# Kernel optimization log

Hardware: AMD Instinct MI355X
Metric: run time of the kernel (lower is better)

## Reference

```python
import jax, jax.numpy as jnp
import numpy as np

B, C_FEAT, C_COND, C_KEY, H, W = 4, 256, 256, 32, 64, 64


def setup_inputs() -> dict:
    key = jax.random.key(0)
    ks = jax.random.split(key, 8)
    s = 0.02
    return {
        "features": jax.random.normal(ks[0], (B, C_FEAT, H, W), jnp.float32),
        "conditions": jax.random.normal(ks[1], (B, C_COND, H, W), jnp.float32),
        "Wq": jax.random.normal(ks[2], (C_KEY, C_COND), jnp.float32) * s,
        "bq": jnp.zeros((C_KEY,), jnp.float32),
        "Wk": jax.random.normal(ks[3], (C_KEY, C_FEAT), jnp.float32) * s,
        "bk": jnp.zeros((C_KEY,), jnp.float32),
        "Wv": jax.random.normal(ks[4], (C_FEAT, C_FEAT), jnp.float32) * s,
        "bv": jnp.zeros((C_FEAT,), jnp.float32),
        "gamma": jnp.zeros((1,), jnp.float32),
    }


def reference(features, conditions, Wq, bq, Wk, bk, Wv, bv, gamma):
    b, c, h, w = features.shape
    n = h * w
    feat = features.reshape(b, c, n)            # [B, C, N]
    cond = conditions.reshape(b, cond_c := conditions.shape[1], n)
    # 1x1 convs == per-pixel linear projections
    q = jnp.einsum('kc,bcn->bnk', Wq, cond) + bq          # [B, N, Ck]
    k = jnp.einsum('kc,bcn->bkn', Wk, feat) + bk[:, None]  # [B, Ck, N]
    v = jnp.einsum('oc,bcn->bon', Wv, feat) + bv[:, None]  # [B, C, N]
    energy = jnp.einsum('bik,bkj->bij', q, k)             # [B, N, N]
    attn = jax.nn.softmax(energy, axis=-1)
    out = jnp.einsum('bcj,bij->bci', v, attn)             # [B, C, N]
    out = out.reshape(b, c, h, w)
    return gamma * out + features
```

## Files before the change

### kernel.cpp

```cpp
#include <hip/hip_runtime.h>

typedef __bf16 bf16_t;
typedef __bf16 bf16x2 __attribute__((ext_vector_type(2)));
typedef __bf16 bf16x4 __attribute__((ext_vector_type(4)));
typedef __bf16 bf16x8 __attribute__((ext_vector_type(8)));
typedef float f32x4 __attribute__((ext_vector_type(4)));
typedef unsigned u32;
typedef unsigned u32x4 __attribute__((ext_vector_type(4)));

#define N_PIX 4096
#define CFEAT 256
#define CKEY 32
#define NBATCH 4

#if __has_builtin(__builtin_amdgcn_exp2f)
#define EXP2(x) __builtin_amdgcn_exp2f(x)
#else
#define EXP2(x) exp2f(x)
#endif

static __device__ __forceinline__ f32x4 mfma16(bf16x8 a, bf16x8 b, f32x4 c) {
    return __builtin_amdgcn_mfma_f32_16x16x32_bf16(a, b, c, 0, 0, 0);
}

static __device__ __forceinline__ void glds16(const void* g, void* l) {
    __builtin_amdgcn_global_load_lds(
        (const __attribute__((address_space(1))) void*)g,
        (__attribute__((address_space(3))) void*)l, 16, 0, 0);
}

static __device__ __forceinline__ u32 pk2(float lo, float hi) {
    bf16x2 t; t[0] = (bf16_t)lo; t[1] = (bf16_t)hi;
    return __builtin_bit_cast(u32, t);
}

static __device__ __forceinline__ void xpose4(u32 &x, u32 &y) {
#if __has_builtin(__builtin_amdgcn_permlane32_swap) && __has_builtin(__builtin_amdgcn_permlane16_swap)
    auto r32 = __builtin_amdgcn_permlane32_swap(x, y, false, false);
    auto r16 = __builtin_amdgcn_permlane16_swap(r32[0], r32[1], false, false);
    x = r16[0]; y = r16[1];
#else
    const int lane = threadIdx.x & 63;
    const int g = lane >> 4, ln = lane & 15;
    const int i0 = ln + ((g & 1) << 5);
    const int i2 = i0 + 16;
    u32 xs0 = (u32)__shfl((int)x, i0), ys0 = (u32)__shfl((int)y, i0);
    u32 xs2 = (u32)__shfl((int)x, i2), ys2 = (u32)__shfl((int)y, i2);
    x = (g < 2) ? xs0 : ys0;
    y = (g < 2) ? xs2 : ys2;
#endif
}

static __device__ __forceinline__ void softmax_tile(
    const bf16x8 kf[4], bf16x8 qf, bool addl,
    float &ls0, float &ls1, float &ls2, float &ls3,
    bf16x8 &pa0, bf16x8 &pa1)
{
    f32x4 zero = {0.f, 0.f, 0.f, 0.f};
    f32x4 st[4];
#pragma unroll
    for (int jt = 0; jt < 4; ++jt) st[jt] = mfma16(kf[jt], qf, zero);
    float ex[16];
#pragma unroll
    for (int jt = 0; jt < 4; ++jt)
#pragma unroll
        for (int r = 0; r < 4; ++r) ex[jt * 4 + r] = EXP2(st[jt][r]);
    if (addl) {
#pragma unroll
        for (int t = 0; t < 16; t += 4) {
            ls0 += ex[t]; ls1 += ex[t + 1]; ls2 += ex[t + 2]; ls3 += ex[t + 3];
        }
    }
    u32 a0 = pk2(ex[0],  ex[1]),  a1 = pk2(ex[2],  ex[3]);
    u32 b0 = pk2(ex[4],  ex[5]),  b1 = pk2(ex[6],  ex[7]);
    u32 c0 = pk2(ex[8],  ex[9]),  c1 = pk2(ex[10], ex[11]);
    u32 d0 = pk2(ex[12], ex[13]), d1 = pk2(ex[14], ex[15]);
    xpose4(a0, b0); xpose4(a1, b1);
    xpose4(c0, d0); xpose4(c1, d1);
    u32x4 w0 = {a0, a1, b0, b1};
    u32x4 w1 = {c0, c1, d0, d1};
    pa0 = __builtin_bit_cast(bf16x8, w0);
    pa1 = __builtin_bit_cast(bf16x8, w1);
}

__global__ __launch_bounds__(256) void projqk_kernel(
    const float* __restrict__ Wq, const float* __restrict__ bq, const float* __restrict__ Xq,
    const float* __restrict__ Wk, const float* __restrict__ bk, const float* __restrict__ Xk,
    bf16_t* __restrict__ Qt, bf16_t* __restrict__ Kt)
{
    __shared__ __attribute__((aligned(16))) bf16_t T[64][40];
    const int lane = threadIdx.x & 63, wave = threadIdx.x >> 6;
    const int g = lane >> 4, ln = lane & 15;
    const bool isK = (blockIdx.y == 1);
    const float* W    = isK ? Wk : Wq;
    const float* bias = isK ? bk : bq;
    const float* X  = (isK ? Xk : Xq) + (size_t)blockIdx.z * CFEAT * N_PIX;
    bf16_t*      Yt = (isK ? Kt : Qt) + (size_t)blockIdx.z * N_PIX * CKEY;
    const float qscale = isK ? 1.0f : 1.4426950408889634f;

    const int m_base = (wave & 1) * 16;
    const int n_loc  = (wave >> 1) * 32;
    const int n_base = blockIdx.x * 64 + n_loc;

    f32x4 zero = {0.f, 0.f, 0.f, 0.f};
    f32x4 acc[2] = {zero, zero};
    for (int k0 = 0; k0 < CFEAT; k0 += 32) {
        bf16x8 a;
        const float* wp = W + (size_t)(m_base + ln) * CFEAT + k0 + g * 8;
#pragma unroll
        for (int j = 0; j < 8; ++j) a[j] = (bf16_t)wp[j];
#pragma unroll
        for (int nt = 0; nt < 2; ++nt) {
            const float* xp = X + (size_t)(k0 + g * 8) * N_PIX + n_base + nt * 16 + ln;
            bf16x8 bfr;
#pragma unroll
            for (int j = 0; j < 8; ++j) bfr[j] = (bf16_t)xp[(size_t)j * N_PIX];
            acc[nt] = mfma16(a, bfr, acc[nt]);
        }
    }
#pragma unroll
    for (int nt = 0; nt < 2; ++nt)
#pragma unroll
        for (int r = 0; r < 4; ++r) {
            const int ck = m_base + g * 4 + r;
            T[n_loc + nt * 16 + ln][ck] = (bf16_t)((acc[nt][r] + bias[ck]) * qscale);
        }
    __syncthreads();
    const int n  = threadIdx.x >> 2;
    const int sg = threadIdx.x & 3;
    bf16x8 row = *(const bf16x8*)&T[n][sg * 8];
    *(bf16x8*)&Yt[(size_t)(blockIdx.x * 64 + n) * CKEY + sg * 8] = row;
}

__global__ __launch_bounds__(256, 4) void projv_kernel(
    const float* __restrict__ W, const float* __restrict__ bias,
    const float* __restrict__ X, bf16_t* __restrict__ V)
{
    const int lane = threadIdx.x & 63, wave = threadIdx.x >> 6;
    const int g = lane >> 4, ln = lane & 15;
    const int b = blockIdx.z;
    const int n_base = blockIdx.x * 32;
    const int c_wave = blockIdx.y * 128 + wave * 32;
    const float* Xb = X + (size_t)b * CFEAT * N_PIX;
    bf16_t*      Vb = V + (size_t)b * CFEAT * N_PIX;

    f32x4 zero = {0.f, 0.f, 0.f, 0.f};
    f32x4 acc[2][2];
#pragma unroll
    for (int mt = 0; mt < 2; ++mt) { acc[mt][0] = zero; acc[mt][1] = zero; }

    for (int k0 = 0; k0 < CFEAT; k0 += 32) {
        bf16x8 bfr[2];
#pragma unroll
        for (int nt = 0; nt < 2; ++nt) {
            const float* xp = Xb + (size_t)(k0 + g * 8) * N_PIX + n_base + nt * 16 + ln;
#pragma unroll
            for (int j = 0; j < 8; ++j) bfr[nt][j] = (bf16_t)xp[(size_t)j * N_PIX];
        }
#pragma unroll
        for (int mt = 0; mt < 2; ++mt) {
            const float* wp = W + (size_t)(c_wave + mt * 16 + ln) * CFEAT + k0 + g * 8;
            bf16x8 a;
#pragma unroll
            for (int j = 0; j < 8; ++j) a[j] = (bf16_t)wp[j];
            acc[mt][0] = mfma16(a, bfr[0], acc[mt][0]);
            acc[mt][1] = mfma16(a, bfr[1], acc[mt][1]);
        }
    }
#pragma unroll
    for (int mt = 0; mt < 2; ++mt)
#pragma unroll
        for (int nt = 0; nt < 2; ++nt)
#pragma unroll
            for (int r = 0; r < 4; ++r) {
                const int m = c_wave + mt * 16 + g * 4 + r;
                const int n = n_base + nt * 16 + ln;
                Vb[(size_t)m * N_PIX + n] = (bf16_t)(acc[mt][nt][r] + bias[m]);
            }
}

__global__ __launch_bounds__(256, 4) void pv_kernel(
    const bf16_t* __restrict__ Qt, const bf16_t* __restrict__ Kt,
    const bf16_t* __restrict__ V,
    const float* __restrict__ features, const float* __restrict__ gamma,
    float* __restrict__ out)
{
    __shared__ __attribute__((aligned(16))) bf16_t Vlds[4][64 * 64];

    const int lane = threadIdx.x & 63, wave = threadIdx.x >> 6;
    const int g = lane >> 4, ln = lane & 15;
    const int b = blockIdx.z;
    const int i_base = blockIdx.y * 64 + wave * 16;
    const int c_base = blockIdx.x * 64;

    const bf16_t* Qb = Qt + (size_t)b * N_PIX * CKEY;
    const bf16_t* Kb = Kt + (size_t)b * N_PIX * CKEY;
    const bf16_t* Vb = V + (size_t)b * CFEAT * N_PIX;

    const int s0 = wave * 128 + lane;
    const int s1 = s0 + 64;
    const int sc0 = s0 >> 3, sj0 = (s0 & 7) ^ (sc0 & 7);
    const int sc1 = s1 >> 3, sj1 = (s1 & 7) ^ (sc1 & 7);
    const bf16_t* vg0 = Vb + (size_t)(c_base + sc0) * N_PIX + sj0 * 8;
    const bf16_t* vg1 = Vb + (size_t)(c_base + sc1) * N_PIX + sj1 * 8;

    const bf16x8 qf = *(const bf16x8*)&Qb[(size_t)(i_base + ln) * CKEY + g * 8];

    f32x4 zero = {0.f, 0.f, 0.f, 0.f};
    f32x4 acc[4] = {zero, zero, zero, zero};
    float ls0 = 0.f, ls1 = 0.f, ls2 = 0.f, ls3 = 0.f;

    bf16x8 pa0c, pa1c;
    {
        bf16x8 kf[4];
#pragma unroll
        for (int jt = 0; jt < 4; ++jt)
            kf[jt] = *(const bf16x8*)&Kb[(size_t)(jt * 16 + ln) * CKEY + g * 8];
        asm volatile("" ::: "memory");
        glds16(vg0,      &Vlds[0][wave * 1024]);
        glds16(vg1,      &Vlds[0][wave * 1024 + 512]);
        glds16(vg0 + 64, &Vlds[1][wave * 1024]);
        glds16(vg1 + 64, &Vlds[1][wave * 1024 + 512]);
        softmax_tile(kf, qf, true, ls0, ls1, ls2, ls3, pa0c, pa1c);
        asm volatile("s_waitcnt vmcnt(2)" ::: "memory");
        __builtin_amdgcn_s_barrier();
        asm volatile("" ::: "memory");
    }

    for (int n = 0; n < 64; ++n) {
        const bf16_t* Vt = &Vlds[n & 3][0];
        bf16x8 vf[8];
#pragma unroll
        for (int ct = 0; ct < 4; ++ct) {
            const int c = ct * 16 + ln;
            vf[2 * ct]     = *(const bf16x8*)&Vt[(c * 8 + ( g      ^ (c & 7))) * 8];
            vf[2 * ct + 1] = *(const bf16x8*)&Vt[(c * 8 + ((4 + g) ^ (c & 7))) * 8];
        }

        const int jq = ((n + 1) & 63) * 64;
        bf16x8 kf[4];
#pragma unroll
        for (int jt = 0; jt < 4; ++jt)
            kf[jt] = *(const bf16x8*)&Kb[(size_t)(jq + jt * 16 + ln) * CKEY + g * 8];
        asm volatile("" ::: "memory");

        const int jn = (n * 64 + 128) & (N_PIX - 1);
        bf16_t* ldst = &Vlds[(n + 2) & 3][wave * 1024];
        glds16(vg0 + jn, ldst);
        glds16(vg1 + jn, ldst + 512);

        bf16x8 pa0n, pa1n;
        softmax_tile(kf, qf, n < 63, ls0, ls1, ls2, ls3, pa0n, pa1n);

        asm volatile("s_waitcnt vmcnt(2)" ::: "memory");
        __builtin_amdgcn_s_barrier();
        asm volatile("" ::: "memory");

#pragma unroll
        for (int ct = 0; ct < 4; ++ct) {
            acc[ct] = mfma16(vf[2 * ct],     pa0c, acc[ct]);
            acc[ct] = mfma16(vf[2 * ct + 1], pa1c, acc[ct]);
        }
        pa0c = pa0n; pa1c = pa1n;
    }

    float lsum = (ls0 + ls1) + (ls2 + ls3);
    lsum += __shfl_xor(lsum, 16);
    lsum += __shfl_xor(lsum, 32);
    const float s_lane = gamma[0] / lsum;

#pragma unroll
    for (int ct = 0; ct < 4; ++ct)
#pragma unroll
        for (int r = 0; r < 4; ++r) {
            const int c = c_base + ct * 16 + g * 4 + r;
            const int i = i_base + ln;
            const size_t idx = ((size_t)b * CFEAT + c) * N_PIX + i;
            out[idx] = s_lane * acc[ct][r] + features[idx];
        }
}

extern "C" void kernel_launch(void* const* d_in, const int* in_sizes, int n_in,
                              void* d_out, int out_size, void* d_ws, size_t ws_size,
                              hipStream_t stream) {
    const float* features   = (const float*)d_in[0];
    const float* conditions = (const float*)d_in[1];
    const float* Wq  = (const float*)d_in[2];
    const float* bq  = (const float*)d_in[3];
    const float* Wk  = (const float*)d_in[4];
    const float* bk  = (const float*)d_in[5];
    const float* Wv  = (const float*)d_in[6];
    const float* bv  = (const float*)d_in[7];
    const float* gam = (const float*)d_in[8];
    float* out = (float*)d_out;

    bf16_t* Qt = (bf16_t*)d_ws;
    bf16_t* Kt = Qt + (size_t)NBATCH * N_PIX * CKEY;
    bf16_t* Vw = Kt + (size_t)NBATCH * N_PIX * CKEY;

    projqk_kernel<<<dim3(N_PIX / 64, 2, NBATCH), 256, 0, stream>>>(
        Wq, bq, conditions, Wk, bk, features, Qt, Kt);
    projv_kernel<<<dim3(N_PIX / 32, 2, NBATCH), 256, 0, stream>>>(Wv, bv, features, Vw);
    pv_kernel<<<dim3(4, N_PIX / 64, NBATCH), 256, 0, stream>>>(
        Qt, Kt, Vw, features, gam, out);
}
```

Measured before the change: 193.0 us.

## Widen PV channel tile to 128, compute row sums via MFMA, double-buffer K loads

Each pv_kernel block now covers 128 channels instead of 64. This halves the number of blocks that recompute the QK^T energies and the exp for the same rows, and the launch grid is halved to match. The softmax denominator now comes from an MFMA against a ones vector on the bf16-packed probabilities rather than scalar float adds. The main loop is unrolled by two, with ping-pong K fragment registers prefetched two tiles ahead. In exchange, register and LDS use double (launch bounds drop to 2 waves per SIMD), and the row sums now use bf16-rounded values.

Measured after the change: 172.8 us. 10.4% less time.

```diff
diff --git a/kernel.cpp b/kernel.cpp
--- a/kernel.cpp
+++ b/kernel.cpp
@@ -52,9 +52,8 @@
 }
 
 static __device__ __forceinline__ void softmax_tile(
-    const bf16x8 kf[4], bf16x8 qf, bool addl,
-    float &ls0, float &ls1, float &ls2, float &ls3,
-    bf16x8 &pa0, bf16x8 &pa1)
+    const bf16x8 kf[4], bf16x8 qf, bf16x8 ones,
+    f32x4 &accsum, bf16x8 &pa0, bf16x8 &pa1)
 {
     f32x4 zero = {0.f, 0.f, 0.f, 0.f};
     f32x4 st[4];
@@ -65,12 +64,6 @@
     for (int jt = 0; jt < 4; ++jt)
 #pragma unroll
         for (int r = 0; r < 4; ++r) ex[jt * 4 + r] = EXP2(st[jt][r]);
-    if (addl) {
-#pragma unroll
-        for (int t = 0; t < 16; t += 4) {
-            ls0 += ex[t]; ls1 += ex[t + 1]; ls2 += ex[t + 2]; ls3 += ex[t + 3];
-        }
-    }
     u32 a0 = pk2(ex[0],  ex[1]),  a1 = pk2(ex[2],  ex[3]);
     u32 b0 = pk2(ex[4],  ex[5]),  b1 = pk2(ex[6],  ex[7]);
     u32 c0 = pk2(ex[8],  ex[9]),  c1 = pk2(ex[10], ex[11]);
@@ -81,6 +74,8 @@
     u32x4 w1 = {c0, c1, d0, d1};
     pa0 = __builtin_bit_cast(bf16x8, w0);
     pa1 = __builtin_bit_cast(bf16x8, w1);
+    accsum = mfma16(ones, pa0, accsum);
+    accsum = mfma16(ones, pa1, accsum);
 }
 
 __global__ __launch_bounds__(256) void projqk_kernel(
@@ -179,98 +174,128 @@
             }
 }
 
-__global__ __launch_bounds__(256, 4) void pv_kernel(
+__global__ __launch_bounds__(256, 2) void pv_kernel(
     const bf16_t* __restrict__ Qt, const bf16_t* __restrict__ Kt,
     const bf16_t* __restrict__ V,
     const float* __restrict__ features, const float* __restrict__ gamma,
     float* __restrict__ out)
 {
-    __shared__ __attribute__((aligned(16))) bf16_t Vlds[4][64 * 64];
+    __shared__ __attribute__((aligned(16))) bf16_t Vlds[4][128 * 64];
 
     const int lane = threadIdx.x & 63, wave = threadIdx.x >> 6;
     const int g = lane >> 4, ln = lane & 15;
     const int b = blockIdx.z;
     const int i_base = blockIdx.y * 64 + wave * 16;
-    const int c_base = blockIdx.x * 64;
+    const int c_base = blockIdx.x * 128;
 
     const bf16_t* Qb = Qt + (size_t)b * N_PIX * CKEY;
     const bf16_t* Kb = Kt + (size_t)b * N_PIX * CKEY;
     const bf16_t* Vb = V + (size_t)b * CFEAT * N_PIX;
 
-    const int s0 = wave * 128 + lane;
-    const int s1 = s0 + 64;
+    const int s0 = wave * 256 + lane, s1 = s0 + 64, s2 = s0 + 128, s3 = s0 + 192;
     const int sc0 = s0 >> 3, sj0 = (s0 & 7) ^ (sc0 & 7);
     const int sc1 = s1 >> 3, sj1 = (s1 & 7) ^ (sc1 & 7);
+    const int sc2 = s2 >> 3, sj2 = (s2 & 7) ^ (sc2 & 7);
+    const int sc3 = s3 >> 3, sj3 = (s3 & 7) ^ (sc3 & 7);
     const bf16_t* vg0 = Vb + (size_t)(c_base + sc0) * N_PIX + sj0 * 8;
     const bf16_t* vg1 = Vb + (size_t)(c_base + sc1) * N_PIX + sj1 * 8;
+    const bf16_t* vg2 = Vb + (size_t)(c_base + sc2) * N_PIX + sj2 * 8;
+    const bf16_t* vg3 = Vb + (size_t)(c_base + sc3) * N_PIX + sj3 * 8;
 
     const bf16x8 qf = *(const bf16x8*)&Qb[(size_t)(i_base + ln) * CKEY + g * 8];
 
+    bf16x8 ones;
+#pragma unroll
+    for (int j = 0; j < 8; ++j) ones[j] = (bf16_t)1.0f;
+
     f32x4 zero = {0.f, 0.f, 0.f, 0.f};
-    f32x4 acc[4] = {zero, zero, zero, zero};
-    float ls0 = 0.f, ls1 = 0.f, ls2 = 0.f, ls3 = 0.f;
-
+    f32x4 acc[8] = {zero, zero, zero, zero, zero, zero, zero, zero};
+    f32x4 accsum = zero;
+
+    bf16x8 kfA[4], kfB[4];
     bf16x8 pa0c, pa1c;
+
     {
-        bf16x8 kf[4];
+        bf16x8 kf0[4];
 #pragma unroll
         for (int jt = 0; jt < 4; ++jt)
-            kf[jt] = *(const bf16x8*)&Kb[(size_t)(jt * 16 + ln) * CKEY + g * 8];
+            kf0[jt] = *(const bf16x8*)&Kb[(size_t)(jt * 16 + ln) * CKEY + g * 8];
         asm volatile("" ::: "memory");
-        glds16(vg0,      &Vlds[0][wave * 1024]);
-        glds16(vg1,      &Vlds[0][wave * 1024 + 512]);
-        glds16(vg0 + 64, &Vlds[1][wave * 1024]);
-        glds16(vg1 + 64, &Vlds[1][wave * 1024 + 512]);
-        softmax_tile(kf, qf, true, ls0, ls1, ls2, ls3, pa0c, pa1c);
-        asm volatile("s_waitcnt vmcnt(2)" ::: "memory");
+        glds16(vg0, &Vlds[0][wave * 2048]);
+        glds16(vg1, &Vlds[0][wave * 2048 + 512]);
+        glds16(vg2, &Vlds[0][wave * 2048 + 1024]);
+        glds16(vg3, &Vlds[0][wave * 2048 + 1536]);
+        glds16(vg0 + 64, &Vlds[1][wave * 2048]);
+        glds16(vg1 + 64, &Vlds[1][wave * 2048 + 512]);
+        glds16(vg2 + 64, &Vlds[1][wave * 2048 + 1024]);
+        glds16(vg3 + 64, &Vlds[1][wave * 2048 + 1536]);
+#pragma unroll
+        for (int jt = 0; jt < 4; ++jt)
+            kfA[jt] = *(const bf16x8*)&Kb[(size_t)(64 + jt * 16 + ln) * CKEY + g * 8];
+        softmax_tile(kf0, qf, ones, accsum, pa0c, pa1c);
+        asm volatile("s_waitcnt vmcnt(8)" ::: "memory");
         __builtin_amdgcn_s_barrier();
         asm volatile("" ::: "memory");
     }
 
-    for (int n = 0; n < 64; ++n) {
-        const bf16_t* Vt = &Vlds[n & 3][0];
-        bf16x8 vf[8];
-#pragma unroll
-        for (int ct = 0; ct < 4; ++ct) {
-            const int c = ct * 16 + ln;
-            vf[2 * ct]     = *(const bf16x8*)&Vt[(c * 8 + ( g      ^ (c & 7))) * 8];
-            vf[2 * ct + 1] = *(const bf16x8*)&Vt[(c * 8 + ((4 + g) ^ (c & 7))) * 8];
-        }
-
-        const int jq = ((n + 1) & 63) * 64;
-        bf16x8 kf[4];
-#pragma unroll
-        for (int jt = 0; jt < 4; ++jt)
-            kf[jt] = *(const bf16x8*)&Kb[(size_t)(jq + jt * 16 + ln) * CKEY + g * 8];
-        asm volatile("" ::: "memory");
-
-        const int jn = (n * 64 + 128) & (N_PIX - 1);
-        bf16_t* ldst = &Vlds[(n + 2) & 3][wave * 1024];
-        glds16(vg0 + jn, ldst);
-        glds16(vg1 + jn, ldst + 512);
-
-        bf16x8 pa0n, pa1n;
-        softmax_tile(kf, qf, n < 63, ls0, ls1, ls2, ls3, pa0n, pa1n);
-
-        asm volatile("s_waitcnt vmcnt(2)" ::: "memory");
-        __builtin_amdgcn_s_barrier();
-        asm volatile("" ::: "memory");
-
-#pragma unroll
-        for (int ct = 0; ct < 4; ++ct) {
-            acc[ct] = mfma16(vf[2 * ct],     pa0c, acc[ct]);
-            acc[ct] = mfma16(vf[2 * ct + 1], pa1c, acc[ct]);
-        }
-        pa0c = pa0n; pa1c = pa1n;
+#define PV_ITER(NN, KFU, KFN)                                                  \
+  {                                                                            \
+    const int nn = (NN);                                                       \
+    const bf16_t* Vt = &Vlds[nn & 3][0];                                       \
+    bf16x8 vfl[8];                                                             \
+    _Pragma("unroll")                                                          \
+    for (int ct = 0; ct < 4; ++ct) {                                           \
+      const int c = ct * 16 + ln;                                              \
+      vfl[2 * ct]     = *(const bf16x8*)&Vt[(c * 8 + ( g      ^ (c & 7))) * 8];\
+      vfl[2 * ct + 1] = *(const bf16x8*)&Vt[(c * 8 + ((4 + g) ^ (c & 7))) * 8];\
+    }                                                                          \
+    const int jq2 = ((nn + 2) & 63) * 64;                                      \
+    _Pragma("unroll")                                                          \
+    for (int jt = 0; jt < 4; ++jt)                                             \
+      KFN[jt] = *(const bf16x8*)&Kb[(size_t)(jq2 + jt * 16 + ln) * CKEY + g * 8]; \
+    asm volatile("" ::: "memory");     \
+    const int jn = (nn * 64 + 128) & (N_PIX - 1);                              \
+    bf16_t* ldst = &Vlds[(nn + 2) & 3][wave * 2048];                           \
+    glds16(vg0 + jn, ldst);                                                    \
+    glds16(vg1 + jn, ldst + 512);                                              \
+    glds16(vg2 + jn, ldst + 1024);                                             \
+    glds16(vg3 + jn, ldst + 1536);                                             \
+    bf16x8 pa0n, pa1n;                                                         \
+    const bool live = (nn < 63);                                               \
+    if (live) softmax_tile(KFU, qf, ones, accsum, pa0n, pa1n);                 \
+    asm volatile("s_waitcnt vmcnt(8)" ::: "memory");                           \
+    __builtin_amdgcn_s_barrier();                                              \
+    asm volatile("" ::: "memory");                                             \
+    bf16x8 vfh[8];                                                             \
+    _Pragma("unroll")                                                          \
+    for (int ct = 4; ct < 8; ++ct) {                                           \
+      const int c = ct * 16 + ln;                                              \
+      vfh[2 * (ct - 4)]     = *(const bf16x8*)&Vt[(c * 8 + ( g      ^ (c & 7))) * 8]; \
+      vfh[2 * (ct - 4) + 1] = *(const bf16x8*)&Vt[(c * 8 + ((4 + g) ^ (c & 7))) * 8]; \
+    }                                                                          \
+    _Pragma("unroll")                                                          \
+    for (int ct = 0; ct < 4; ++ct) {                                           \
+      acc[ct] = mfma16(vfl[2 * ct],     pa0c, acc[ct]);                        \
+      acc[ct] = mfma16(vfl[2 * ct + 1], pa1c, acc[ct]);                        \
+    }                                                                          \
+    _Pragma("unroll")                                                          \
+    for (int ct = 0; ct < 4; ++ct) {                                           \
+      acc[4 + ct] = mfma16(vfh[2 * ct],     pa0c, acc[4 + ct]);                \
+      acc[4 + ct] = mfma16(vfh[2 * ct + 1], pa1c, acc[4 + ct]);                \
+    }                                                                          \
+    if (live) { pa0c = pa0n; pa1c = pa1n; }                                    \
+  }
+
+    for (int n2 = 0; n2 < 32; ++n2) {
+        PV_ITER(2 * n2,     kfA, kfB);
+        PV_ITER(2 * n2 + 1, kfB, kfA);
     }
-
-    float lsum = (ls0 + ls1) + (ls2 + ls3);
-    lsum += __shfl_xor(lsum, 16);
-    lsum += __shfl_xor(lsum, 32);
-    const float s_lane = gamma[0] / lsum;
-
-#pragma unroll
-    for (int ct = 0; ct < 4; ++ct)
+#undef PV_ITER
+
+    const float s_lane = gamma[0] / accsum[0];
+
+#pragma unroll
+    for (int ct = 0; ct < 8; ++ct)
 #pragma unroll
         for (int r = 0; r < 4; ++r) {
             const int c = c_base + ct * 16 + g * 4 + r;
@@ -301,6 +326,6 @@
     projqk_kernel<<<dim3(N_PIX / 64, 2, NBATCH), 256, 0, stream>>>(
         Wq, bq, conditions, Wk, bk, features, Qt, Kt);
     projv_kernel<<<dim3(N_PIX / 32, 2, NBATCH), 256, 0, stream>>>(Wv, bv, features, Vw);
-    pv_kernel<<<dim3(4, N_PIX / 64, NBATCH), 256, 0, stream>>>(
+    pv_kernel<<<dim3(2, N_PIX / 64, NBATCH), 256, 0, stream>>>(
         Qt, Kt, Vw, features, gam, out);
 }
```
